# Performance work log

Hardware: AMD Instinct MI355X
Metric: run time of the kernel (lower is better)

## Reference

```python
import jax, jax.numpy as jnp
import numpy as np

C = 256; G = 16; GC = C // G; K = 3; P = K * K
N = 4; H = 64; W = 64
PAD = 1; OFFSET_SCALE = 1.0; LN_EPS = 1e-5


def setup_inputs() -> dict:
    key = jax.random.key(0)
    ks = jax.random.split(key, 8)
    s = 0.02
    return {
        "x": jax.random.normal(ks[0], (N, C, H, W), jnp.float32),
        "dw_w": jax.random.normal(ks[1], (C, 1, K, K), jnp.float32) * s,
        "dw_b": jnp.zeros((C,), jnp.float32),
        "ln_g": jnp.ones((C,), jnp.float32),
        "ln_b": jnp.zeros((C,), jnp.float32),
        "off_w": jax.random.normal(ks[2], (C, G * P * 2), jnp.float32) * s,
        "off_b": jnp.zeros((G * P * 2,), jnp.float32),
        "mask_w": jax.random.normal(ks[3], (C, G * P), jnp.float32) * s,
        "mask_b": jnp.zeros((G * P,), jnp.float32),
        "inp_w": jax.random.normal(ks[4], (C, C), jnp.float32) * s,
        "inp_b": jnp.zeros((C,), jnp.float32),
        "out_w": jax.random.normal(ks[5], (C, C), jnp.float32) * s,
        "out_b": jnp.zeros((C,), jnp.float32),
    }


def _dcnv3_nchw(x, dw_w, dw_b, ln_g, ln_b, off_w, off_b, mask_w, mask_b,
                inp_w, inp_b, out_w, out_b):
    # NCHW -> NHWC (wrapper permute)
    xn = jnp.transpose(x, (0, 2, 3, 1))                      # (N,H,W,C)
    x_proj = xn @ inp_w + inp_b                              # input_proj

    # offset/mask branch: depthwise conv (NCHW) -> LayerNorm (channels-last) -> GELU
    x1 = jax.lax.conv_general_dilated(
        x, dw_w, window_strides=(1, 1), padding=((PAD, PAD), (PAD, PAD)),
        dimension_numbers=("NCHW", "OIHW", "NCHW"), feature_group_count=C)
    x1 = jnp.transpose(x1, (0, 2, 3, 1)) + dw_b
    mu = x1.mean(-1, keepdims=True)
    var = ((x1 - mu) ** 2).mean(-1, keepdims=True)
    x1 = (x1 - mu) * jax.lax.rsqrt(var + LN_EPS) * ln_g + ln_b
    x1 = jax.nn.gelu(x1, approximate=False)

    offset = (x1 @ off_w + off_b).reshape(N, H, W, G, P, 2)  # (x,y) pairs
    mask = jax.nn.softmax((x1 @ mask_w + mask_b).reshape(N, H, W, G, P), axis=-1)

    # pad sampled feature map with zeros (F.pad before sampling)
    xp = jnp.pad(x_proj, ((0, 0), (PAD, PAD), (PAD, PAD), (0, 0)))
    Hin, Win = H + 2 * PAD, W + 2 * PAD
    xg = xp.reshape(N, Hin, Win, G, GC)

    # reference points, normalized by padded size
    ref_y = (jnp.arange(H, dtype=jnp.float32) + PAD + 0.5) / Hin
    ref_x = (jnp.arange(W, dtype=jnp.float32) + PAD + 0.5) / Win
    ref = jnp.stack([jnp.broadcast_to(ref_x[None, :], (H, W)),
                     jnp.broadcast_to(ref_y[:, None], (H, W))], -1)  # (H,W,2)

    # dilation grid: x varies in the outer loop (torch meshgrid 'ij')
    d = jnp.arange(K, dtype=jnp.float32) - (K - 1) // 2     # [-1,0,1]
    gx = jnp.repeat(d, K) / Win
    gy = jnp.tile(d, K) / Hin
    grid = jnp.stack([gx, gy], -1)                           # (P,2)

    norm = jnp.array([Win, Hin], jnp.float32)
    loc = (ref[None, :, :, None, None, :] + grid * OFFSET_SCALE
           + offset * OFFSET_SCALE / norm)                   # (N,H,W,G,P,2)

    # grid_sample bilinear, align_corners=False, zero padding
    px = loc[..., 0] * Win - 0.5
    py = loc[..., 1] * Hin - 0.5
    x0 = jnp.floor(px); y0 = jnp.floor(py)
    wx = px - x0; wy = py - y0
    x0i = x0.astype(jnp.int32); y0i = y0.astype(jnp.int32)

    n_idx = jnp.arange(N)[:, None, None, None, None]
    g_idx = jnp.arange(G)[None, None, None, :, None]

    def corner(iy, ix, w):
        valid = (iy >= 0) & (iy < Hin) & (ix >= 0) & (ix < Win)
        v = xg[n_idx, jnp.clip(iy, 0, Hin - 1), jnp.clip(ix, 0, Win - 1), g_idx]
        wgt = jnp.where(valid, w, 0.0) * mask                # fold mask into weights
        return jnp.einsum("nhwgp,nhwgpc->nhwgc", wgt, v)

    out = (corner(y0i, x0i, (1 - wy) * (1 - wx))
           + corner(y0i, x0i + 1, (1 - wy) * wx)
           + corner(y0i + 1, x0i, wy * (1 - wx))
           + corner(y0i + 1, x0i + 1, wy * wx))               # (N,H,W,G,GC)

    out = out.reshape(N, H, W, C) @ out_w + out_b            # output_proj
    return jnp.transpose(out, (0, 3, 1, 2))                  # NHWC -> NCHW


def reference(x, dw_w, dw_b, ln_g, ln_b, off_w, off_b, mask_w, mask_b,
              inp_w, inp_b, out_w, out_b):
    return _dcnv3_nchw(x, dw_w, dw_b, ln_g, ln_b, off_w, off_b,
                       mask_w, mask_b, inp_w, inp_b, out_w, out_b)
```

## Files before the change

kernel.cpp:

```cpp
#include <hip/hip_runtime.h>
#include <hip/hip_bf16.h>
#include <math.h>


using bf16x8 = __attribute__((ext_vector_type(8))) short;
using f32x4  = __attribute__((ext_vector_type(4))) float;

#define GLOBAL_AS __attribute__((address_space(1)))
#define LDS_AS    __attribute__((address_space(3)))

static __device__ inline void g2lds16(const void* g, void* l) {
  __builtin_amdgcn_global_load_lds((const GLOBAL_AS int*)g, (LDS_AS int*)l, 16, 0, 0);
}
static __device__ inline unsigned short f2bf(float v) {
  __hip_bfloat16 b = __float2bfloat16(v);
  return *reinterpret_cast<unsigned short*>(&b);
}
static __device__ inline float us2f(unsigned short u) {
  union { unsigned u; float f; } c; c.u = ((unsigned)u) << 16; return c.f;
}

__global__ __launch_bounds__(256) void prep_k(
    const float* __restrict__ inp_w, const float* __restrict__ off_w,
    const float* __restrict__ off_b, const float* __restrict__ mask_w,
    const float* __restrict__ mask_b, const float* __restrict__ out_w,
    __hip_bfloat16* __restrict__ BtI, __hip_bfloat16* __restrict__ BtOM,
    __hip_bfloat16* __restrict__ BtO, float* __restrict__ bOM)
{
  int b = blockIdx.x, t = threadIdx.x;
  if (b < 256) {
    int n = b;
    BtI[n * 256 + t] = __float2bfloat16(inp_w[t * 256 + n]);
  } else if (b < 768) {
    int n = b - 256;
    float v = 0.f;
    if (n < 288) v = off_w[t * 288 + n];
    else if (n < 432) v = mask_w[t * 144 + (n - 288)];
    BtOM[n * 256 + t] = __float2bfloat16(v);
    if (b == 256) {
      for (int idx = t; idx < 512; idx += 256) {
        float bv = (idx < 288) ? off_b[idx] : ((idx < 432) ? mask_b[idx - 288] : 0.f);
        bOM[idx] = bv;
      }
    }
  } else {
    int n = b - 768;
    BtO[n * 256 + t] = __float2bfloat16(out_w[t * 256 + n]);
  }
}

__global__ __launch_bounds__(256) void xt_k(const float* __restrict__ x,
                                            __hip_bfloat16* __restrict__ xT) {
  __shared__ float tile[32][65];
  const int hw0 = blockIdx.x * 64, c0 = blockIdx.y * 32, n4 = blockIdx.z;
  const int t = threadIdx.x;
  #pragma unroll
  for (int r = 0; r < 8; ++r) {
    int idx = t + r * 256;
    int cl = idx >> 6, wl = idx & 63;
    tile[cl][wl] = x[(size_t)n4 * 1048576 + (size_t)(c0 + cl) * 4096 + hw0 + wl];
  }
  __syncthreads();
  #pragma unroll
  for (int r = 0; r < 2; ++r) {
    int idx = t + r * 256;
    int pixl = idx >> 3, cq = idx & 7;
    unsigned short b0 = f2bf(tile[cq * 4 + 0][pixl]);
    unsigned short b1 = f2bf(tile[cq * 4 + 1][pixl]);
    unsigned short b2 = f2bf(tile[cq * 4 + 2][pixl]);
    unsigned short b3 = f2bf(tile[cq * 4 + 3][pixl]);
    uint2 u;
    u.x = (unsigned)b0 | ((unsigned)b1 << 16);
    u.y = (unsigned)b2 | ((unsigned)b3 << 16);
    *(uint2*)&xT[((size_t)n4 * 4096 + hw0 + pixl) * 256 + c0 + cq * 4] = u;
  }
}

template<int CMODE>
__global__ __launch_bounds__(256) void gemm_mfma(
    const __hip_bfloat16* __restrict__ A, const __hip_bfloat16* __restrict__ Bt,
    const float* __restrict__ bias, void* __restrict__ Cv, int ldc, int nstore)
{
  __shared__ __align__(16) char smem[16512];
  short* As = (short*)smem;
  short* Bs = (short*)(smem + 8192);
  float* tb = (float*)smem;
  const int t = threadIdx.x;
  const int wave = t >> 6, lane = t & 63;
  const int quad = lane >> 4, lr = lane & 15;
  const int wm = wave >> 1, wn = wave & 1;
  const size_t m0 = (size_t)blockIdx.y * 128;
  const int n0 = blockIdx.x * 128;

  f32x4 acc[4][4];
  #pragma unroll
  for (int i = 0; i < 4; ++i)
    #pragma unroll
    for (int j = 0; j < 4; ++j)
      acc[i][j] = (f32x4){0.f, 0.f, 0.f, 0.f};

  const int srow = wave * 32;
  for (int kt = 0; kt < 256; kt += 32) {
    #pragma unroll
    for (int j = 0; j < 2; ++j) {
      int chunk = j * 64 + lane;
      int row = srow + (chunk >> 2), kq = chunk & 3;
      const __hip_bfloat16* gA = A + (m0 + row) * 256 + kt + kq * 8;
      const __hip_bfloat16* gB = Bt + (size_t)(n0 + row) * 256 + kt + kq * 8;
      g2lds16(gA, (char*)As + wave * 2048 + j * 1024);
      g2lds16(gB, (char*)Bs + wave * 2048 + j * 1024);
    }
    __syncthreads();
    bf16x8 bfv[4];
    #pragma unroll
    for (int ni = 0; ni < 4; ++ni)
      bfv[ni] = *(const bf16x8*)&Bs[(wn * 64 + ni * 16 + lr) * 32 + quad * 8];
    #pragma unroll
    for (int mi = 0; mi < 4; ++mi) {
      bf16x8 af = *(const bf16x8*)&As[(wm * 64 + mi * 16 + lr) * 32 + quad * 8];
      #pragma unroll
      for (int ni = 0; ni < 4; ++ni)
        acc[mi][ni] = __builtin_amdgcn_mfma_f32_16x16x32_bf16(af, bfv[ni], acc[mi][ni], 0, 0, 0);
    }
    __syncthreads();
  }

  if (CMODE == 2) {
    #pragma unroll
    for (int mi = 0; mi < 4; ++mi) {
      #pragma unroll
      for (int ni = 0; ni < 4; ++ni) {
        int col = n0 + wn * 64 + ni * 16 + lr;
        if (col < nstore) {
          float bv = bias[col];
          #pragma unroll
          for (int reg = 0; reg < 4; ++reg) {
            size_t m = m0 + wm * 64 + mi * 16 + quad * 4 + reg;
            ((__hip_bfloat16*)Cv)[m * ldc + col] =
                __float2bfloat16(acc[mi][ni][reg] + bv);
          }
        }
      }
    }
  } else {
    const int n4 = (int)(m0 >> 12), hw0 = (int)(m0 & 4095);
    for (int qc = 0; qc < 4; ++qc) {
      __syncthreads();
      if (wn == (qc >> 1)) {
        #pragma unroll
        for (int nis = 0; nis < 2; ++nis) {
          int ni = 2 * (qc & 1) + nis;
          int col = n0 + wn * 64 + ni * 16 + lr;
          float bv = bias[col];
          int cl = nis * 16 + lr;
          #pragma unroll
          for (int mi = 0; mi < 4; ++mi)
            #pragma unroll
            for (int reg = 0; reg < 4; ++reg) {
              int ml = wm * 64 + mi * 16 + quad * 4 + reg;
              tb[cl * 129 + ml] = acc[mi][ni][reg] + bv;
            }
        }
      }
      __syncthreads();
      #pragma unroll
      for (int r = 0; r < 4; ++r) {
        int f4i = t + r * 256;
        int row = f4i >> 5, mc = (f4i & 31) * 4;
        int co = n0 + qc * 32 + row;
        float4 v;
        v.x = tb[row * 129 + mc + 0];
        v.y = tb[row * 129 + mc + 1];
        v.z = tb[row * 129 + mc + 2];
        v.w = tb[row * 129 + mc + 3];
        *(float4*)&((float*)Cv)[(size_t)(n4 * 256 + co) * 4096 + hw0 + mc] = v;
      }
    }
  }
}

__global__ __launch_bounds__(256) void dwconv_k(
    const float* __restrict__ x, const float* __restrict__ dw_w,
    const float* __restrict__ dw_b, float* __restrict__ y)
{
  __shared__ float pl[4096];
  const int bc = blockIdx.x;
  const int n4 = bc >> 8, c = bc & 255;
  const int t = threadIdx.x;
  const float* xc = x + (size_t)n4 * 1048576 + (size_t)c * 4096;
  #pragma unroll
  for (int r = 0; r < 4; ++r) {
    int idx4 = t + r * 256;
    *(float4*)&pl[idx4 * 4] = *(const float4*)&xc[idx4 * 4];
  }
  float wv[9];
  #pragma unroll
  for (int i = 0; i < 9; ++i) wv[i] = dw_w[c * 9 + i];
  const float bb = dw_b[c];
  __syncthreads();
  float* yc = y + (size_t)(n4 * 256 + c) * 4096;
  #pragma unroll 4
  for (int r = 0; r < 16; ++r) {
    int px = t + r * 256;
    int h = px >> 6, w = px & 63;
    float s = bb;
    #pragma unroll
    for (int dh = -1; dh <= 1; ++dh) {
      int hh = h + dh;
      if ((unsigned)hh >= 64u) continue;
      #pragma unroll
      for (int dw = -1; dw <= 1; ++dw) {
        int ww = w + dw;
        if ((unsigned)ww >= 64u) continue;
        s = fmaf(pl[hh * 64 + ww], wv[(dh + 1) * 3 + (dw + 1)], s);
      }
    }
    yc[px] = s;
  }
}

__global__ __launch_bounds__(256) void ln_k(
    const float* __restrict__ y, const float* __restrict__ ln_g,
    const float* __restrict__ ln_b, __hip_bfloat16* __restrict__ x1)
{
  __shared__ float ps[4][64], pq[4][64], mu_s[64], rs_s[64];
  __shared__ unsigned short st[256 * 65];
  const int blk = blockIdx.x;
  const int n4 = blk >> 6, h = blk & 63;
  const int t = threadIdx.x;
  const int w = t & 63, cq = t >> 6;
  const float* yb = y + (size_t)n4 * 1048576 + h * 64 + w;
  float v[64];
  float s1 = 0.f, s2 = 0.f;
  #pragma unroll
  for (int i = 0; i < 64; ++i) {
    v[i] = yb[(size_t)(cq * 64 + i) * 4096];
    s1 += v[i];
    s2 = fmaf(v[i], v[i], s2);
  }
  ps[cq][w] = s1; pq[cq][w] = s2;
  __syncthreads();
  if (t < 64) {
    float a = ps[0][t] + ps[1][t] + ps[2][t] + ps[3][t];
    float b = pq[0][t] + pq[1][t] + pq[2][t] + pq[3][t];
    float mu = a * (1.f / 256.f);
    mu_s[t] = mu;
    rs_s[t] = rsqrtf(b * (1.f / 256.f) - mu * mu + 1e-5f);
  }
  __syncthreads();
  const float mu = mu_s[w], rs = rs_s[w];
  #pragma unroll
  for (int i = 0; i < 64; ++i) {
    int c = cq * 64 + i;
    float yv = fmaf((v[i] - mu) * rs, ln_g[c], ln_b[c]);
    float ge = 0.5f * yv * (1.f + erff(yv * 0.70710678f));
    st[c * 65 + w] = f2bf(ge);
  }
  __syncthreads();
  const size_t row0 = (size_t)n4 * 4096 + (size_t)h * 64;
  #pragma unroll
  for (int r = 0; r < 16; ++r) {
    int idx = t + r * 256;
    int pix = idx >> 6, cq4 = idx & 63;
    unsigned short b0 = st[(cq4 * 4 + 0) * 65 + pix];
    unsigned short b1 = st[(cq4 * 4 + 1) * 65 + pix];
    unsigned short b2 = st[(cq4 * 4 + 2) * 65 + pix];
    unsigned short b3 = st[(cq4 * 4 + 3) * 65 + pix];
    uint2 u;
    u.x = (unsigned)b0 | ((unsigned)b1 << 16);
    u.y = (unsigned)b2 | ((unsigned)b3 << 16);
    *(uint2*)&x1[(row0 + pix) * 256 + cq4 * 4] = u;
  }
}

__global__ __launch_bounds__(256) void sample_k(
    const __hip_bfloat16* __restrict__ xpu, const __hip_bfloat16* __restrict__ om,
    __hip_bfloat16* __restrict__ samp)
{
  __shared__ unsigned short oms[16 * 448];
  const int bid = blockIdx.x;
  const int region = bid & 7;
  const int q = bid >> 3;
  const int pix0 = region * 2048 + q * 16;
  const int t = threadIdx.x;

  {
    const uint4* gsrc = (const uint4*)(om + (size_t)pix0 * 448);
    uint4* ldst = (uint4*)oms;
    #pragma unroll
    for (int r = 0; r < 4; ++r) {
      int i = t + r * 256;
      if (i < 896) ldst[i] = gsrc[i];
    }
  }
  __syncthreads();

  const int g = t & 15;
  const int pl = t >> 4;
  const int pix = pix0 + pl;
  const int n4 = pix >> 12;
  const int hw = pix & 4095;
  const int h = hw >> 6, w = hw & 63;

  float mk[9];
  {
    const unsigned short* mp = &oms[pl * 448 + 288 + g * 9];
    float mx = -1e30f;
    #pragma unroll
    for (int p = 0; p < 9; ++p) { mk[p] = us2f(mp[p]); mx = fmaxf(mx, mk[p]); }
    float se = 0.f;
    #pragma unroll
    for (int p = 0; p < 9; ++p) { mk[p] = __expf(mk[p] - mx); se += mk[p]; }
    float inv = 1.f / se;
    #pragma unroll
    for (int p = 0; p < 9; ++p) mk[p] *= inv;
  }

  const unsigned short* op = &oms[pl * 448 + g * 18];
  const __hip_bfloat16* xpg = xpu + (g << 4);
  float ax[16];
  #pragma unroll
  for (int i = 0; i < 16; ++i) ax[i] = 0.f;

  auto corner = [&](int iy, int ix, float wt) {
    if ((unsigned)(iy - 1) >= 64u || (unsigned)(ix - 1) >= 64u) return;
    const __hip_bfloat16* src =
        xpg + ((size_t)((n4 << 12) + (iy - 1) * 64 + (ix - 1)) << 8);
    uint4 u0 = *(const uint4*)src;
    uint4 u1 = *(const uint4*)(src + 8);
    const unsigned uu[8] = {u0.x, u0.y, u0.z, u0.w, u1.x, u1.y, u1.z, u1.w};
    #pragma unroll
    for (int i = 0; i < 8; ++i) {
      float lo = us2f((unsigned short)(uu[i] & 0xffff));
      float hi = us2f((unsigned short)(uu[i] >> 16));
      ax[2 * i + 0] = fmaf(wt, lo, ax[2 * i + 0]);
      ax[2 * i + 1] = fmaf(wt, hi, ax[2 * i + 1]);
    }
  };

  #pragma unroll
  for (int p = 0; p < 9; ++p) {
    float ox = us2f(op[2 * p]), oy = us2f(op[2 * p + 1]);
    float px = (float)(w + p / 3) + ox;
    float py = (float)(h + p % 3) + oy;
    float xf = floorf(px), yf = floorf(py);
    float wx = px - xf, wy = py - yf;
    int ix = (int)xf, iy = (int)yf;
    float m = mk[p];
    corner(iy,     ix,     (1.f - wy) * (1.f - wx) * m);
    corner(iy,     ix + 1, (1.f - wy) * wx * m);
    corner(iy + 1, ix,     wy * (1.f - wx) * m);
    corner(iy + 1, ix + 1, wy * wx * m);
  }

  unsigned short ub[16];
  #pragma unroll
  for (int i = 0; i < 16; ++i) ub[i] = f2bf(ax[i]);
  uint4* d4 = (uint4*)(samp + (size_t)pix * 256 + (g << 4));
  uint4 u0, u1;
  u0.x = (unsigned)ub[0] | ((unsigned)ub[1] << 16);
  u0.y = (unsigned)ub[2] | ((unsigned)ub[3] << 16);
  u0.z = (unsigned)ub[4] | ((unsigned)ub[5] << 16);
  u0.w = (unsigned)ub[6] | ((unsigned)ub[7] << 16);
  u1.x = (unsigned)ub[8] | ((unsigned)ub[9] << 16);
  u1.y = (unsigned)ub[10] | ((unsigned)ub[11] << 16);
  u1.z = (unsigned)ub[12] | ((unsigned)ub[13] << 16);
  u1.w = (unsigned)ub[14] | ((unsigned)ub[15] << 16);
  d4[0] = u0; d4[1] = u1;
}

extern "C" void kernel_launch(void* const* d_in, const int* in_sizes, int n_in,
                              void* d_out, int out_size, void* d_ws, size_t ws_size,
                              hipStream_t stream) {
  const float* x      = (const float*)d_in[0];
  const float* dw_w   = (const float*)d_in[1];
  const float* dw_b   = (const float*)d_in[2];
  const float* ln_g   = (const float*)d_in[3];
  const float* ln_b   = (const float*)d_in[4];
  const float* off_w  = (const float*)d_in[5];
  const float* off_b  = (const float*)d_in[6];
  const float* mask_w = (const float*)d_in[7];
  const float* mask_b = (const float*)d_in[8];
  const float* inp_w  = (const float*)d_in[9];
  const float* inp_b  = (const float*)d_in[10];
  const float* out_w  = (const float*)d_in[11];
  const float* out_b  = (const float*)d_in[12];
  float* out = (float*)d_out;

  char* w0 = (char*)d_ws;
  __hip_bfloat16* xpu  = (__hip_bfloat16*)(w0);
  float*          y    = (float*)(w0 + 8388608);
  __hip_bfloat16* x1   = (__hip_bfloat16*)(w0 + 25165824);
  __hip_bfloat16* xT   = (__hip_bfloat16*)(w0 + 33554432);
  __hip_bfloat16* samp = xT;
  __hip_bfloat16* om   = (__hip_bfloat16*)(w0 + 41943040);
  __hip_bfloat16* BtI  = (__hip_bfloat16*)(w0 + 56623104);
  __hip_bfloat16* BtOM = (__hip_bfloat16*)(w0 + 56754176);
  __hip_bfloat16* BtO  = (__hip_bfloat16*)(w0 + 57016320);
  float*          bOM  = (float*)(w0 + 57147392);
  if (ws_size < 57149440) return;

  prep_k<<<1024, 256, 0, stream>>>(inp_w, off_w, off_b, mask_w, mask_b, out_w,
                                   BtI, BtOM, BtO, bOM);
  xt_k<<<dim3(64, 8, 4), 256, 0, stream>>>(x, xT);
  gemm_mfma<2><<<dim3(2, 128), 256, 0, stream>>>(xT, BtI, inp_b, xpu, 256, 256);
  dwconv_k<<<1024, 256, 0, stream>>>(x, dw_w, dw_b, y);
  ln_k<<<256, 256, 0, stream>>>(y, ln_g, ln_b, x1);
  gemm_mfma<2><<<dim3(4, 128), 256, 0, stream>>>(x1, BtOM, bOM, om, 448, 432);
  sample_k<<<1024, 256, 0, stream>>>(xpu, om, samp);
  gemm_mfma<3><<<dim3(2, 128), 256, 0, stream>>>(samp, BtO, out_b, out, 0, 256);
}
```

Baseline: 181.9 us.

## Fuse transpose into input GEMM, fuse sampling with output projection, bf16 dwconv output

The separate NCHW-to-NHWC transpose kernel is removed. The input-projection GEMM now loads fp32 x directly into LDS and converts it to bf16 while building its A fragments. The sampling kernel and the output-projection GEMM are merged into one kernel: sampled values stay in LDS and feed MFMA directly, and the result is written transposed to NCHW, which removes one global round trip. The depthwise-conv intermediate is stored as bf16 to halve its traffic. The costs are strided LDS reads with per-element conversion in the GEMM, fewer and heavier blocks in the fused kernel (512 blocks of 32 pixels each reloading BtO), and lower precision for the LN input.

```diff
diff --git a/kernel.cpp b/kernel.cpp
--- a/kernel.cpp
+++ b/kernel.cpp
@@ -49,48 +49,24 @@
   }
 }
 
-__global__ __launch_bounds__(256) void xt_k(const float* __restrict__ x,
-                                            __hip_bfloat16* __restrict__ xT) {
-  __shared__ float tile[32][65];
-  const int hw0 = blockIdx.x * 64, c0 = blockIdx.y * 32, n4 = blockIdx.z;
-  const int t = threadIdx.x;
-  #pragma unroll
-  for (int r = 0; r < 8; ++r) {
-    int idx = t + r * 256;
-    int cl = idx >> 6, wl = idx & 63;
-    tile[cl][wl] = x[(size_t)n4 * 1048576 + (size_t)(c0 + cl) * 4096 + hw0 + wl];
-  }
-  __syncthreads();
-  #pragma unroll
-  for (int r = 0; r < 2; ++r) {
-    int idx = t + r * 256;
-    int pixl = idx >> 3, cq = idx & 7;
-    unsigned short b0 = f2bf(tile[cq * 4 + 0][pixl]);
-    unsigned short b1 = f2bf(tile[cq * 4 + 1][pixl]);
-    unsigned short b2 = f2bf(tile[cq * 4 + 2][pixl]);
-    unsigned short b3 = f2bf(tile[cq * 4 + 3][pixl]);
-    uint2 u;
-    u.x = (unsigned)b0 | ((unsigned)b1 << 16);
-    u.y = (unsigned)b2 | ((unsigned)b3 << 16);
-    *(uint2*)&xT[((size_t)n4 * 4096 + hw0 + pixl) * 256 + c0 + cq * 4] = u;
-  }
-}
-
-template<int CMODE>
+template<int ASRC>
 __global__ __launch_bounds__(256) void gemm_mfma(
-    const __hip_bfloat16* __restrict__ A, const __hip_bfloat16* __restrict__ Bt,
-    const float* __restrict__ bias, void* __restrict__ Cv, int ldc, int nstore)
+    const void* __restrict__ Av, const __hip_bfloat16* __restrict__ Bt,
+    const float* __restrict__ bias, __hip_bfloat16* __restrict__ C,
+    int ldc, int nstore)
 {
-  __shared__ __align__(16) char smem[16512];
-  short* As = (short*)smem;
-  short* Bs = (short*)(smem + 8192);
-  float* tb = (float*)smem;
+  constexpr int ABYTES = ASRC ? 16384 : 8192;
+  __shared__ __align__(16) char smem[ABYTES + 8192];
+  short* As  = (short*)smem;
+  float* Asf = (float*)smem;
+  short* Bs  = (short*)(smem + ABYTES);
   const int t = threadIdx.x;
   const int wave = t >> 6, lane = t & 63;
   const int quad = lane >> 4, lr = lane & 15;
   const int wm = wave >> 1, wn = wave & 1;
   const size_t m0 = (size_t)blockIdx.y * 128;
   const int n0 = blockIdx.x * 128;
+  const int n4 = (int)(m0 >> 12), hw0 = (int)(m0 & 4095);
 
   f32x4 acc[4][4];
   #pragma unroll
@@ -99,16 +75,34 @@
     for (int j = 0; j < 4; ++j)
       acc[i][j] = (f32x4){0.f, 0.f, 0.f, 0.f};
 
-  const int srow = wave * 32;
   for (int kt = 0; kt < 256; kt += 32) {
-    #pragma unroll
-    for (int j = 0; j < 2; ++j) {
-      int chunk = j * 64 + lane;
-      int row = srow + (chunk >> 2), kq = chunk & 3;
-      const __hip_bfloat16* gA = A + (m0 + row) * 256 + kt + kq * 8;
-      const __hip_bfloat16* gB = Bt + (size_t)(n0 + row) * 256 + kt + kq * 8;
-      g2lds16(gA, (char*)As + wave * 2048 + j * 1024);
-      g2lds16(gB, (char*)Bs + wave * 2048 + j * 1024);
+    if (ASRC == 0) {
+      const __hip_bfloat16* A = (const __hip_bfloat16*)Av;
+      #pragma unroll
+      for (int j = 0; j < 2; ++j) {
+        int chunk = j * 64 + lane;
+        int row = wave * 32 + (chunk >> 2), kq = chunk & 3;
+        g2lds16(A + (m0 + row) * 256 + kt + kq * 8,
+                (char*)As + wave * 2048 + j * 1024 + (lane & 63) * 16 - lane * 16 + lane * 16);
+      }
+    } else {
+      const float* X = (const float*)Av;
+      #pragma unroll
+      for (int j = 0; j < 4; ++j) {
+        int krow = wave * 8 + j * 2 + (lane >> 5);
+        int px4 = (lane & 31) * 4;
+        g2lds16(X + (size_t)n4 * 1048576 + (size_t)(kt + krow) * 4096 + hw0 + px4,
+                (char*)smem + wave * 4096 + j * 1024 + lane * 16);
+      }
+    }
+    {
+      #pragma unroll
+      for (int j = 0; j < 2; ++j) {
+        int chunk = j * 64 + lane;
+        int row = wave * 32 + (chunk >> 2), kq = chunk & 3;
+        g2lds16(Bt + (size_t)(n0 + row) * 256 + kt + kq * 8,
+                (char*)Bs + wave * 2048 + j * 1024 + lane * 16);
+      }
     }
     __syncthreads();
     bf16x8 bfv[4];
@@ -117,7 +111,15 @@
       bfv[ni] = *(const bf16x8*)&Bs[(wn * 64 + ni * 16 + lr) * 32 + quad * 8];
     #pragma unroll
     for (int mi = 0; mi < 4; ++mi) {
-      bf16x8 af = *(const bf16x8*)&As[(wm * 64 + mi * 16 + lr) * 32 + quad * 8];
+      bf16x8 af;
+      if (ASRC == 0) {
+        af = *(const bf16x8*)&As[(wm * 64 + mi * 16 + lr) * 32 + quad * 8];
+      } else {
+        int m = wm * 64 + mi * 16 + lr;
+        #pragma unroll
+        for (int j2 = 0; j2 < 8; ++j2)
+          ((unsigned short*)&af)[j2] = f2bf(Asf[(quad * 8 + j2) * 128 + m]);
+      }
       #pragma unroll
       for (int ni = 0; ni < 4; ++ni)
         acc[mi][ni] = __builtin_amdgcn_mfma_f32_16x16x32_bf16(af, bfv[ni], acc[mi][ni], 0, 0, 0);
@@ -125,55 +127,18 @@
     __syncthreads();
   }
 
-  if (CMODE == 2) {
-    #pragma unroll
-    for (int mi = 0; mi < 4; ++mi) {
-      #pragma unroll
-      for (int ni = 0; ni < 4; ++ni) {
-        int col = n0 + wn * 64 + ni * 16 + lr;
-        if (col < nstore) {
-          float bv = bias[col];
-          #pragma unroll
-          for (int reg = 0; reg < 4; ++reg) {
-            size_t m = m0 + wm * 64 + mi * 16 + quad * 4 + reg;
-            ((__hip_bfloat16*)Cv)[m * ldc + col] =
-                __float2bfloat16(acc[mi][ni][reg] + bv);
-          }
+  #pragma unroll
+  for (int mi = 0; mi < 4; ++mi) {
+    #pragma unroll
+    for (int ni = 0; ni < 4; ++ni) {
+      int col = n0 + wn * 64 + ni * 16 + lr;
+      if (col < nstore) {
+        float bv = bias[col];
+        #pragma unroll
+        for (int reg = 0; reg < 4; ++reg) {
+          size_t m = m0 + wm * 64 + mi * 16 + quad * 4 + reg;
+          C[m * ldc + col] = __float2bfloat16(acc[mi][ni][reg] + bv);
         }
-      }
-    }
-  } else {
-    const int n4 = (int)(m0 >> 12), hw0 = (int)(m0 & 4095);
-    for (int qc = 0; qc < 4; ++qc) {
-      __syncthreads();
-      if (wn == (qc >> 1)) {
-        #pragma unroll
-        for (int nis = 0; nis < 2; ++nis) {
-          int ni = 2 * (qc & 1) + nis;
-          int col = n0 + wn * 64 + ni * 16 + lr;
-          float bv = bias[col];
-          int cl = nis * 16 + lr;
-          #pragma unroll
-          for (int mi = 0; mi < 4; ++mi)
-            #pragma unroll
-            for (int reg = 0; reg < 4; ++reg) {
-              int ml = wm * 64 + mi * 16 + quad * 4 + reg;
-              tb[cl * 129 + ml] = acc[mi][ni][reg] + bv;
-            }
-        }
-      }
-      __syncthreads();
-      #pragma unroll
-      for (int r = 0; r < 4; ++r) {
-        int f4i = t + r * 256;
-        int row = f4i >> 5, mc = (f4i & 31) * 4;
-        int co = n0 + qc * 32 + row;
-        float4 v;
-        v.x = tb[row * 129 + mc + 0];
-        v.y = tb[row * 129 + mc + 1];
-        v.z = tb[row * 129 + mc + 2];
-        v.w = tb[row * 129 + mc + 3];
-        *(float4*)&((float*)Cv)[(size_t)(n4 * 256 + co) * 4096 + hw0 + mc] = v;
       }
     }
   }
@@ -181,7 +146,7 @@
 
 __global__ __launch_bounds__(256) void dwconv_k(
     const float* __restrict__ x, const float* __restrict__ dw_w,
-    const float* __restrict__ dw_b, float* __restrict__ y)
+    const float* __restrict__ dw_b, __hip_bfloat16* __restrict__ y)
 {
   __shared__ float pl[4096];
   const int bc = blockIdx.x;
@@ -198,7 +163,7 @@
   for (int i = 0; i < 9; ++i) wv[i] = dw_w[c * 9 + i];
   const float bb = dw_b[c];
   __syncthreads();
-  float* yc = y + (size_t)(n4 * 256 + c) * 4096;
+  __hip_bfloat16* yc = y + (size_t)(n4 * 256 + c) * 4096;
   #pragma unroll 4
   for (int r = 0; r < 16; ++r) {
     int px = t + r * 256;
@@ -215,12 +180,12 @@
         s = fmaf(pl[hh * 64 + ww], wv[(dh + 1) * 3 + (dw + 1)], s);
       }
     }
-    yc[px] = s;
+    yc[px] = __float2bfloat16(s);
   }
 }
 
 __global__ __launch_bounds__(256) void ln_k(
-    const float* __restrict__ y, const float* __restrict__ ln_g,
+    const __hip_bfloat16* __restrict__ y, const float* __restrict__ ln_g,
     const float* __restrict__ ln_b, __hip_bfloat16* __restrict__ x1)
 {
   __shared__ float ps[4][64], pq[4][64], mu_s[64], rs_s[64];
@@ -229,12 +194,12 @@
   const int n4 = blk >> 6, h = blk & 63;
   const int t = threadIdx.x;
   const int w = t & 63, cq = t >> 6;
-  const float* yb = y + (size_t)n4 * 1048576 + h * 64 + w;
+  const __hip_bfloat16* yb = y + (size_t)n4 * 1048576 + h * 64 + w;
   float v[64];
   float s1 = 0.f, s2 = 0.f;
   #pragma unroll
   for (int i = 0; i < 64; ++i) {
-    v[i] = yb[(size_t)(cq * 64 + i) * 4096];
+    v[i] = __bfloat162float(yb[(size_t)(cq * 64 + i) * 4096]);
     s1 += v[i];
     s2 = fmaf(v[i], v[i], s2);
   }
@@ -273,100 +238,163 @@
   }
 }
 
-__global__ __launch_bounds__(256) void sample_k(
+__global__ __launch_bounds__(256) void fused_out(
     const __hip_bfloat16* __restrict__ xpu, const __hip_bfloat16* __restrict__ om,
-    __hip_bfloat16* __restrict__ samp)
+    const __hip_bfloat16* __restrict__ BtO, const float* __restrict__ out_b,
+    float* __restrict__ out)
 {
-  __shared__ unsigned short oms[16 * 448];
+  __shared__ __align__(16) char smem[62464];
+  unsigned short* oms = (unsigned short*)smem;
+  short* sampS = (short*)(smem + 29184);
+  short* BsS   = (short*)(smem + 46080);
+  float* tb    = (float*)smem;
+
+  const int t = threadIdx.x;
   const int bid = blockIdx.x;
-  const int region = bid & 7;
-  const int q = bid >> 3;
-  const int pix0 = region * 2048 + q * 16;
-  const int t = threadIdx.x;
+  const int region = bid & 7, qb = bid >> 3;
+  const int pix0 = region * 2048 + qb * 32;
+  const int n4 = pix0 >> 12;
+  const int hw0 = pix0 & 4095;
 
   {
     const uint4* gsrc = (const uint4*)(om + (size_t)pix0 * 448);
-    uint4* ldst = (uint4*)oms;
-    #pragma unroll
-    for (int r = 0; r < 4; ++r) {
-      int i = t + r * 256;
-      if (i < 896) ldst[i] = gsrc[i];
-    }
-  }
-  __syncthreads();
-
-  const int g = t & 15;
-  const int pl = t >> 4;
-  const int pix = pix0 + pl;
-  const int n4 = pix >> 12;
-  const int hw = pix & 4095;
-  const int h = hw >> 6, w = hw & 63;
-
-  float mk[9];
-  {
-    const unsigned short* mp = &oms[pl * 448 + 288 + g * 9];
+    uint4* dst = (uint4*)oms;
+    #pragma unroll
+    for (int k = 0; k < 7; ++k) {
+      int i = t + k * 256;
+      int row = i / 56, col = i - row * 56;
+      dst[row * 57 + col] = gsrc[i];
+    }
+  }
+  __syncthreads();
+
+  #pragma unroll
+  for (int pass = 0; pass < 2; ++pass) {
+    int id = t + pass * 256;
+    int g = id & 15, pl = id >> 4;
+    int hw = hw0 + pl;
+    int h = hw >> 6, w = hw & 63;
+    const unsigned short* ob = &oms[pl * 456];
+
+    float mk[9];
     float mx = -1e30f;
     #pragma unroll
-    for (int p = 0; p < 9; ++p) { mk[p] = us2f(mp[p]); mx = fmaxf(mx, mk[p]); }
+    for (int p = 0; p < 9; ++p) { mk[p] = us2f(ob[288 + g * 9 + p]); mx = fmaxf(mx, mk[p]); }
     float se = 0.f;
     #pragma unroll
     for (int p = 0; p < 9; ++p) { mk[p] = __expf(mk[p] - mx); se += mk[p]; }
     float inv = 1.f / se;
-    #pragma unroll
-    for (int p = 0; p < 9; ++p) mk[p] *= inv;
-  }
-
-  const unsigned short* op = &oms[pl * 448 + g * 18];
-  const __hip_bfloat16* xpg = xpu + (g << 4);
-  float ax[16];
-  #pragma unroll
-  for (int i = 0; i < 16; ++i) ax[i] = 0.f;
-
-  auto corner = [&](int iy, int ix, float wt) {
-    if ((unsigned)(iy - 1) >= 64u || (unsigned)(ix - 1) >= 64u) return;
-    const __hip_bfloat16* src =
-        xpg + ((size_t)((n4 << 12) + (iy - 1) * 64 + (ix - 1)) << 8);
-    uint4 u0 = *(const uint4*)src;
-    uint4 u1 = *(const uint4*)(src + 8);
-    const unsigned uu[8] = {u0.x, u0.y, u0.z, u0.w, u1.x, u1.y, u1.z, u1.w};
-    #pragma unroll
-    for (int i = 0; i < 8; ++i) {
-      float lo = us2f((unsigned short)(uu[i] & 0xffff));
-      float hi = us2f((unsigned short)(uu[i] >> 16));
-      ax[2 * i + 0] = fmaf(wt, lo, ax[2 * i + 0]);
-      ax[2 * i + 1] = fmaf(wt, hi, ax[2 * i + 1]);
-    }
-  };
-
-  #pragma unroll
-  for (int p = 0; p < 9; ++p) {
-    float ox = us2f(op[2 * p]), oy = us2f(op[2 * p + 1]);
-    float px = (float)(w + p / 3) + ox;
-    float py = (float)(h + p % 3) + oy;
-    float xf = floorf(px), yf = floorf(py);
-    float wx = px - xf, wy = py - yf;
-    int ix = (int)xf, iy = (int)yf;
-    float m = mk[p];
-    corner(iy,     ix,     (1.f - wy) * (1.f - wx) * m);
-    corner(iy,     ix + 1, (1.f - wy) * wx * m);
-    corner(iy + 1, ix,     wy * (1.f - wx) * m);
-    corner(iy + 1, ix + 1, wy * wx * m);
-  }
-
-  unsigned short ub[16];
-  #pragma unroll
-  for (int i = 0; i < 16; ++i) ub[i] = f2bf(ax[i]);
-  uint4* d4 = (uint4*)(samp + (size_t)pix * 256 + (g << 4));
-  uint4 u0, u1;
-  u0.x = (unsigned)ub[0] | ((unsigned)ub[1] << 16);
-  u0.y = (unsigned)ub[2] | ((unsigned)ub[3] << 16);
-  u0.z = (unsigned)ub[4] | ((unsigned)ub[5] << 16);
-  u0.w = (unsigned)ub[6] | ((unsigned)ub[7] << 16);
-  u1.x = (unsigned)ub[8] | ((unsigned)ub[9] << 16);
-  u1.y = (unsigned)ub[10] | ((unsigned)ub[11] << 16);
-  u1.z = (unsigned)ub[12] | ((unsigned)ub[13] << 16);
-  u1.w = (unsigned)ub[14] | ((unsigned)ub[15] << 16);
-  d4[0] = u0; d4[1] = u1;
+
+    const __hip_bfloat16* xpg = xpu + (g << 4);
+    float ax[16];
+    #pragma unroll
+    for (int i = 0; i < 16; ++i) ax[i] = 0.f;
+
+    auto corner = [&](int iy, int ix, float wt) {
+      if ((unsigned)(iy - 1) >= 64u || (unsigned)(ix - 1) >= 64u) return;
+      const __hip_bfloat16* src =
+          xpg + ((size_t)((n4 << 12) + (iy - 1) * 64 + (ix - 1)) << 8);
+      uint4 u0 = *(const uint4*)src;
+      uint4 u1 = *(const uint4*)(src + 8);
+      const unsigned uu[8] = {u0.x, u0.y, u0.z, u0.w, u1.x, u1.y, u1.z, u1.w};
+      #pragma unroll
+      for (int i = 0; i < 8; ++i) {
+        float lo = us2f((unsigned short)(uu[i] & 0xffff));
+        float hi = us2f((unsigned short)(uu[i] >> 16));
+        ax[2 * i + 0] = fmaf(wt, lo, ax[2 * i + 0]);
+        ax[2 * i + 1] = fmaf(wt, hi, ax[2 * i + 1]);
+      }
+    };
+
+    #pragma unroll
+    for (int p = 0; p < 9; ++p) {
+      float ox = us2f(ob[2 * (g * 9 + p)]), oy = us2f(ob[2 * (g * 9 + p) + 1]);
+      float px = (float)(w + p / 3) + ox;
+      float py = (float)(h + p % 3) + oy;
+      float xf = floorf(px), yf = floorf(py);
+      float wx = px - xf, wy = py - yf;
+      int ix = (int)xf, iy = (int)yf;
+      float m = mk[p] * inv;
+      corner(iy,     ix,     (1.f - wy) * (1.f - wx) * m);
+      corner(iy,     ix + 1, (1.f - wy) * wx * m);
+      corner(iy + 1, ix,     wy * (1.f - wx) * m);
+      corner(iy + 1, ix + 1, wy * wx * m);
+    }
+
+    unsigned short ub[16];
+    #pragma unroll
+    for (int i = 0; i < 16; ++i) ub[i] = f2bf(ax[i]);
+    uint4 u0, u1;
+    u0.x = (unsigned)ub[0] | ((unsigned)ub[1] << 16);
+    u0.y = (unsigned)ub[2] | ((unsigned)ub[3] << 16);
+    u0.z = (unsigned)ub[4] | ((unsigned)ub[5] << 16);
+    u0.w = (unsigned)ub[6] | ((unsigned)ub[7] << 16);
+    u1.x = (unsigned)ub[8] | ((unsigned)ub[9] << 16);
+    u1.y = (unsigned)ub[10] | ((unsigned)ub[11] << 16);
+    u1.z = (unsigned)ub[12] | ((unsigned)ub[13] << 16);
+    u1.w = (unsigned)ub[14] | ((unsigned)ub[15] << 16);
+    *(uint4*)&sampS[pl * 264 + g * 16] = u0;
+    *(uint4*)&sampS[pl * 264 + g * 16 + 8] = u1;
+  }
+  __syncthreads();
+
+  const int wave = t >> 6, lane = t & 63;
+  const int quad = lane >> 4, lr = lane & 15;
+  f32x4 acc[2][4];
+  #pragma unroll
+  for (int i = 0; i < 2; ++i)
+    #pragma unroll
+    for (int j = 0; j < 4; ++j)
+      acc[i][j] = (f32x4){0.f, 0.f, 0.f, 0.f};
+
+  for (int kt = 0; kt < 256; kt += 32) {
+    #pragma unroll
+    for (int j = 0; j < 4; ++j) {
+      int row = wave * 64 + j * 16 + (lane >> 2), kq = lane & 3;
+      g2lds16(BtO + (size_t)row * 256 + kt + kq * 8,
+              (char*)BsS + wave * 4096 + j * 1024 + lane * 16);
+    }
+    __syncthreads();
+    bf16x8 bfv[4];
+    #pragma unroll
+    for (int ni = 0; ni < 4; ++ni)
+      bfv[ni] = *(const bf16x8*)&BsS[(wave * 64 + ni * 16 + lr) * 32 + quad * 8];
+    #pragma unroll
+    for (int mi = 0; mi < 2; ++mi) {
+      bf16x8 af = *(const bf16x8*)&sampS[(mi * 16 + lr) * 264 + kt + quad * 8];
+      #pragma unroll
+      for (int ni = 0; ni < 4; ++ni)
+        acc[mi][ni] = __builtin_amdgcn_mfma_f32_16x16x32_bf16(af, bfv[ni], acc[mi][ni], 0, 0, 0);
+    }
+    __syncthreads();
+  }
+
+  for (int qc = 0; qc < 8; ++qc) {
+    __syncthreads();
+    if (wave == (qc >> 1)) {
+      #pragma unroll
+      for (int s = 0; s < 2; ++s) {
+        int ni = (qc & 1) * 2 + s;
+        int col = wave * 64 + ni * 16 + lr;
+        float bv = out_b[col];
+        int cl = s * 16 + lr;
+        #pragma unroll
+        for (int mi = 0; mi < 2; ++mi)
+          #pragma unroll
+          for (int reg = 0; reg < 4; ++reg)
+            tb[cl * 33 + mi * 16 + quad * 4 + reg] = acc[mi][ni][reg] + bv;
+      }
+    }
+    __syncthreads();
+    int row = t >> 3, mc = (t & 7) * 4;
+    int co = qc * 32 + row;
+    float4 v;
+    v.x = tb[row * 33 + mc + 0];
+    v.y = tb[row * 33 + mc + 1];
+    v.z = tb[row * 33 + mc + 2];
+    v.w = tb[row * 33 + mc + 3];
+    *(float4*)&out[(size_t)(n4 * 256 + co) * 4096 + hw0 + mc] = v;
+  }
 }
 
 extern "C" void kernel_launch(void* const* d_in, const int* in_sizes, int n_in,
@@ -389,24 +417,20 @@
 
   char* w0 = (char*)d_ws;
   __hip_bfloat16* xpu  = (__hip_bfloat16*)(w0);
-  float*          y    = (float*)(w0 + 8388608);
-  __hip_bfloat16* x1   = (__hip_bfloat16*)(w0 + 25165824);
-  __hip_bfloat16* xT   = (__hip_bfloat16*)(w0 + 33554432);
-  __hip_bfloat16* samp = xT;
-  __hip_bfloat16* om   = (__hip_bfloat16*)(w0 + 41943040);
-  __hip_bfloat16* BtI  = (__hip_bfloat16*)(w0 + 56623104);
-  __hip_bfloat16* BtOM = (__hip_bfloat16*)(w0 + 56754176);
-  __hip_bfloat16* BtO  = (__hip_bfloat16*)(w0 + 57016320);
-  float*          bOM  = (float*)(w0 + 57147392);
-  if (ws_size < 57149440) return;
+  __hip_bfloat16* y    = (__hip_bfloat16*)(w0 + 8388608);
+  __hip_bfloat16* x1   = (__hip_bfloat16*)(w0 + 16777216);
+  __hip_bfloat16* om   = (__hip_bfloat16*)(w0 + 25165824);
+  __hip_bfloat16* BtI  = (__hip_bfloat16*)(w0 + 39845888);
+  __hip_bfloat16* BtOM = (__hip_bfloat16*)(w0 + 39976960);
+  __hip_bfloat16* BtO  = (__hip_bfloat16*)(w0 + 40239104);
+  float*          bOM  = (float*)(w0 + 40370176);
+  if (ws_size < 40372224) return;
 
   prep_k<<<1024, 256, 0, stream>>>(inp_w, off_w, off_b, mask_w, mask_b, out_w,
                                    BtI, BtOM, BtO, bOM);
-  xt_k<<<dim3(64, 8, 4), 256, 0, stream>>>(x, xT);
-  gemm_mfma<2><<<dim3(2, 128), 256, 0, stream>>>(xT, BtI, inp_b, xpu, 256, 256);
+  gemm_mfma<1><<<dim3(2, 128), 256, 0, stream>>>(x, BtI, inp_b, xpu, 256, 256);
   dwconv_k<<<1024, 256, 0, stream>>>(x, dw_w, dw_b, y);
   ln_k<<<256, 256, 0, stream>>>(y, ln_g, ln_b, x1);
-  gemm_mfma<2><<<dim3(4, 128), 256, 0, stream>>>(x1, BtOM, bOM, om, 448, 432);
-  sample_k<<<1024, 256, 0, stream>>>(xpu, om, samp);
-  gemm_mfma<3><<<dim3(2, 128), 256, 0, stream>>>(samp, BtO, out_b, out, 0, 256);
-}
+  gemm_mfma<0><<<dim3(4, 128), 256, 0, stream>>>(x1, BtOM, bOM, om, 448, 432);
+  fused_out<<<512, 256, 0, stream>>>(xpu, om, BtO, out_b, out);
+}
```

After: 200.8 us. +10.4%, slower.

## Store depthwise conv output in bf16 and stage LayerNorm input through LDS

Applied to the files above, without the earlier changes.

The depthwise conv intermediate is now written as bf16 instead of fp32, halving the traffic written by dwconv_k and read back by ln_k. ln_k is restructured to load its row tile into LDS with 16-byte vector loads, cache gamma and beta in LDS, reuse the same buffer for the GELU output, and write x1 with 16-byte stores instead of 8-byte ones. The workspace layout shrinks to match. The cost is an extra rounding step before the LayerNorm statistics, which adds precision risk.

```diff
diff --git a/kernel.cpp b/kernel.cpp
--- a/kernel.cpp
+++ b/kernel.cpp
@@ -181,7 +181,7 @@
 
 __global__ __launch_bounds__(256) void dwconv_k(
     const float* __restrict__ x, const float* __restrict__ dw_w,
-    const float* __restrict__ dw_b, float* __restrict__ y)
+    const float* __restrict__ dw_b, __hip_bfloat16* __restrict__ y)
 {
   __shared__ float pl[4096];
   const int bc = blockIdx.x;
@@ -198,7 +198,7 @@
   for (int i = 0; i < 9; ++i) wv[i] = dw_w[c * 9 + i];
   const float bb = dw_b[c];
   __syncthreads();
-  float* yc = y + (size_t)(n4 * 256 + c) * 4096;
+  __hip_bfloat16* yc = y + (size_t)(n4 * 256 + c) * 4096;
   #pragma unroll 4
   for (int r = 0; r < 16; ++r) {
     int px = t + r * 256;
@@ -215,30 +215,44 @@
         s = fmaf(pl[hh * 64 + ww], wv[(dh + 1) * 3 + (dw + 1)], s);
       }
     }
-    yc[px] = s;
+    yc[px] = __float2bfloat16(s);
   }
 }
 
 __global__ __launch_bounds__(256) void ln_k(
-    const float* __restrict__ y, const float* __restrict__ ln_g,
+    const __hip_bfloat16* __restrict__ y, const float* __restrict__ ln_g,
     const float* __restrict__ ln_b, __hip_bfloat16* __restrict__ x1)
 {
+  __shared__ unsigned short ys[256 * 66];
+  __shared__ float gs[256], bs2[256];
   __shared__ float ps[4][64], pq[4][64], mu_s[64], rs_s[64];
-  __shared__ unsigned short st[256 * 65];
   const int blk = blockIdx.x;
   const int n4 = blk >> 6, h = blk & 63;
   const int t = threadIdx.x;
-  const int w = t & 63, cq = t >> 6;
-  const float* yb = y + (size_t)n4 * 1048576 + h * 64 + w;
-  float v[64];
-  float s1 = 0.f, s2 = 0.f;
-  #pragma unroll
-  for (int i = 0; i < 64; ++i) {
-    v[i] = yb[(size_t)(cq * 64 + i) * 4096];
-    s1 += v[i];
-    s2 = fmaf(v[i], v[i], s2);
-  }
-  ps[cq][w] = s1; pq[cq][w] = s2;
+
+  gs[t] = ln_g[t]; bs2[t] = ln_b[t];
+
+  const __hip_bfloat16* yb = y + (size_t)n4 * 1048576 + h * 64;
+  #pragma unroll
+  for (int r = 0; r < 8; ++r) {
+    int idx = t + r * 256;
+    int c = idx >> 3, w8 = idx & 7;
+    uint4 u = *(const uint4*)(yb + (size_t)c * 4096 + w8 * 8);
+    unsigned* d = (unsigned*)&ys[c * 66 + w8 * 8];
+    d[0] = u.x; d[1] = u.y; d[2] = u.z; d[3] = u.w;
+  }
+  __syncthreads();
+
+  const int w = t & 63, q = t >> 6;
+  {
+    float s1 = 0.f, s2 = 0.f;
+    #pragma unroll
+    for (int i = 0; i < 64; ++i) {
+      float v = us2f(ys[(q * 64 + i) * 66 + w]);
+      s1 += v; s2 = fmaf(v, v, s2);
+    }
+    ps[q][w] = s1; pq[q][w] = s2;
+  }
   __syncthreads();
   if (t < 64) {
     float a = ps[0][t] + ps[1][t] + ps[2][t] + ps[3][t];
@@ -248,28 +262,37 @@
     rs_s[t] = rsqrtf(b * (1.f / 256.f) - mu * mu + 1e-5f);
   }
   __syncthreads();
+
   const float mu = mu_s[w], rs = rs_s[w];
   #pragma unroll
   for (int i = 0; i < 64; ++i) {
-    int c = cq * 64 + i;
-    float yv = fmaf((v[i] - mu) * rs, ln_g[c], ln_b[c]);
+    int c = q * 64 + i;
+    float v = us2f(ys[c * 66 + w]);
+    float yv = fmaf((v - mu) * rs, gs[c], bs2[c]);
     float ge = 0.5f * yv * (1.f + erff(yv * 0.70710678f));
-    st[c * 65 + w] = f2bf(ge);
-  }
-  __syncthreads();
-  const size_t row0 = (size_t)n4 * 4096 + (size_t)h * 64;
-  #pragma unroll
-  for (int r = 0; r < 16; ++r) {
+    ys[c * 66 + w] = f2bf(ge);
+  }
+  __syncthreads();
+
+  const size_t row0 = ((size_t)n4 * 4096 + (size_t)h * 64) * 256;
+  #pragma unroll
+  for (int r = 0; r < 8; ++r) {
     int idx = t + r * 256;
-    int pix = idx >> 6, cq4 = idx & 63;
-    unsigned short b0 = st[(cq4 * 4 + 0) * 65 + pix];
-    unsigned short b1 = st[(cq4 * 4 + 1) * 65 + pix];
-    unsigned short b2 = st[(cq4 * 4 + 2) * 65 + pix];
-    unsigned short b3 = st[(cq4 * 4 + 3) * 65 + pix];
-    uint2 u;
-    u.x = (unsigned)b0 | ((unsigned)b1 << 16);
-    u.y = (unsigned)b2 | ((unsigned)b3 << 16);
-    *(uint2*)&x1[(row0 + pix) * 256 + cq4 * 4] = u;
+    int pix = idx >> 5, co8 = idx & 31;
+    unsigned short v0 = ys[(co8 * 8 + 0) * 66 + pix];
+    unsigned short v1 = ys[(co8 * 8 + 1) * 66 + pix];
+    unsigned short v2 = ys[(co8 * 8 + 2) * 66 + pix];
+    unsigned short v3 = ys[(co8 * 8 + 3) * 66 + pix];
+    unsigned short v4 = ys[(co8 * 8 + 4) * 66 + pix];
+    unsigned short v5 = ys[(co8 * 8 + 5) * 66 + pix];
+    unsigned short v6 = ys[(co8 * 8 + 6) * 66 + pix];
+    unsigned short v7 = ys[(co8 * 8 + 7) * 66 + pix];
+    uint4 u;
+    u.x = (unsigned)v0 | ((unsigned)v1 << 16);
+    u.y = (unsigned)v2 | ((unsigned)v3 << 16);
+    u.z = (unsigned)v4 | ((unsigned)v5 << 16);
+    u.w = (unsigned)v6 | ((unsigned)v7 << 16);
+    *(uint4*)&x1[row0 + (size_t)pix * 256 + co8 * 8] = u;
   }
 }
 
@@ -389,16 +412,16 @@
 
   char* w0 = (char*)d_ws;
   __hip_bfloat16* xpu  = (__hip_bfloat16*)(w0);
-  float*          y    = (float*)(w0 + 8388608);
-  __hip_bfloat16* x1   = (__hip_bfloat16*)(w0 + 25165824);
-  __hip_bfloat16* xT   = (__hip_bfloat16*)(w0 + 33554432);
+  __hip_bfloat16* y    = (__hip_bfloat16*)(w0 + 8388608);
+  __hip_bfloat16* x1   = (__hip_bfloat16*)(w0 + 16777216);
+  __hip_bfloat16* xT   = (__hip_bfloat16*)(w0 + 25165824);
   __hip_bfloat16* samp = xT;
-  __hip_bfloat16* om   = (__hip_bfloat16*)(w0 + 41943040);
-  __hip_bfloat16* BtI  = (__hip_bfloat16*)(w0 + 56623104);
-  __hip_bfloat16* BtOM = (__hip_bfloat16*)(w0 + 56754176);
-  __hip_bfloat16* BtO  = (__hip_bfloat16*)(w0 + 57016320);
-  float*          bOM  = (float*)(w0 + 57147392);
-  if (ws_size < 57149440) return;
+  __hip_bfloat16* om   = (__hip_bfloat16*)(w0 + 33554432);
+  __hip_bfloat16* BtI  = (__hip_bfloat16*)(w0 + 48234496);
+  __hip_bfloat16* BtOM = (__hip_bfloat16*)(w0 + 48365568);
+  __hip_bfloat16* BtO  = (__hip_bfloat16*)(w0 + 48627712);
+  float*          bOM  = (float*)(w0 + 48758784);
+  if (ws_size < 48760832) return;
 
   prep_k<<<1024, 256, 0, stream>>>(inp_w, off_w, off_b, mask_w, mask_b, out_w,
                                    BtI, BtOM, BtO, bOM);
```

Result: no change. 184.1 us (+1.2%).
